# Optimization experiments

Hardware: AMD Instinct MI355X
Metric: run time of the kernel (lower is better)

## Reference

```python
import jax, jax.numpy as jnp
import numpy as np

IMAGE_C = 1
IMAGE_W = 28
PIXELS_PER_ROW = IMAGE_W * IMAGE_C  # 28

B, T, E = 16, IMAGE_W * IMAGE_W * IMAGE_C, 512  # T = 784
H = 8
D = E // H  # head_dim = 64


def get_2d_causal_bias(T):
    idx = jnp.arange(T)
    i = idx // PIXELS_PER_ROW          # row index
    j = (idx % PIXELS_PER_ROW) // IMAGE_C  # col index
    c = idx % IMAGE_C                  # channel index
    q_i, k_i = i[:, None], i[None, :]
    q_j, k_j = j[:, None], j[None, :]
    q_c, k_c = c[:, None], c[None, :]
    allowed = (k_i < q_i) | ((k_i == q_i) & (k_j < q_j)) | (
        (k_i == q_i) & (k_j == q_j) & (k_c <= q_c))
    bias = jnp.where(allowed, 0.0, -jnp.inf).astype(jnp.float32)
    return bias[None, None]  # [1, 1, T, T]


def setup_inputs() -> dict:
    key = jax.random.key(0)
    ks = jax.random.split(key, 5)
    s = 1.0 / np.sqrt(E)
    return {
        "x": jax.random.normal(ks[0], (B, T, E), dtype=jnp.float32),
        "Wq": jax.random.normal(ks[1], (E, E), dtype=jnp.float32) * s,
        "bq": jnp.zeros((E,), dtype=jnp.float32),
        "Wk": jax.random.normal(ks[2], (E, E), dtype=jnp.float32) * s,
        "bk": jnp.zeros((E,), dtype=jnp.float32),
        "Wv": jax.random.normal(ks[3], (E, E), dtype=jnp.float32) * s,
        "bv": jnp.zeros((E,), dtype=jnp.float32),
        "Wo": jax.random.normal(ks[4], (E, E), dtype=jnp.float32) * s,
        "bo": jnp.zeros((E,), dtype=jnp.float32),
    }


def reference(x, Wq, bq, Wk, bk, Wv, bv, Wo, bo):
    Bx, Tx, Ex = x.shape
    # projections (torch Linear: y = x @ W.T + b; here W stored as [E, E] used directly)
    Q = (x @ Wq + bq).reshape(Bx, Tx, H, D).transpose(0, 2, 1, 3)  # [B,H,T,D]
    K = (x @ Wk + bk).reshape(Bx, Tx, H, D).transpose(0, 2, 1, 3)
    V = (x @ Wv + bv).reshape(Bx, Tx, H, D).transpose(0, 2, 1, 3)
    scores = jnp.einsum("bhqd,bhkd->bhqk", Q, K) / jnp.sqrt(jnp.float32(D))
    scores = scores + get_2d_causal_bias(Tx)
    attn = jax.nn.softmax(scores, axis=-1)
    ctx = jnp.einsum("bhqk,bhkd->bhqd", attn, V)
    ctx = ctx.transpose(0, 2, 1, 3).reshape(Bx, Tx, Ex)
    return ctx @ Wo + bo
```

## Files before the change

kernel.cpp:

```cpp
#include <hip/hip_runtime.h>
#include <hip/hip_bf16.h>

#define BB    16
#define TT    784
#define TPK   832
#define TPQ   896
#define EE    512
#define HH    8
#define DD    64
#define BT    (BB*TT)

typedef short short8 __attribute__((ext_vector_type(8)));
typedef short short4v __attribute__((ext_vector_type(4)));
typedef float floatx4 __attribute__((ext_vector_type(4)));
typedef float floatx16 __attribute__((ext_vector_type(16)));
typedef unsigned uint4v __attribute__((ext_vector_type(4)));

__device__ __forceinline__ short f2bf(float f) {
    unsigned u = __builtin_bit_cast(unsigned, f);
    u += 0x7FFFu + ((u >> 16) & 1u);
    return (short)(u >> 16);
}

__device__ __forceinline__ unsigned cvtpk_bf16(float lo, float hi) {
    unsigned r;
    asm("v_cvt_pk_bf16_f32 %0, %1, %2" : "=v"(r) : "v"(lo), "v"(hi));
    return r;
}

__device__ __forceinline__ void gload_lds16(const short* g, short* l) {
    __builtin_amdgcn_global_load_lds(
        (const __attribute__((address_space(1))) void*)g,
        (__attribute__((address_space(3))) void*)l, 16, 0, 0);
}

__global__ void prep_kernel(const float* __restrict__ x, short* __restrict__ xb,
                            const float* __restrict__ Wq, const float* __restrict__ Wk,
                            const float* __restrict__ Wv, short* __restrict__ wqkvt,
                            const float* __restrict__ Wo, short* __restrict__ wot,
                            short* __restrict__ Qb, short* __restrict__ Kb, short* __restrict__ Vt)
{
    __shared__ short t[64][65];
    int b = blockIdx.x;
    if (b < 3136) {
        int i = (b * 256 + threadIdx.x) * 8;
        float4 a = *(const float4*)(x + i);
        float4 c = *(const float4*)(x + i + 4);
        short8 o;
        o[0] = f2bf(a.x); o[1] = f2bf(a.y); o[2] = f2bf(a.z); o[3] = f2bf(a.w);
        o[4] = f2bf(c.x); o[5] = f2bf(c.y); o[6] = f2bf(c.z); o[7] = f2bf(c.w);
        *(short8*)(xb + i) = o;
    } else if (b < 3392) {
        const float* W; short* out; int n0, k0;
        if (b < 3328) {
            int tt = b - 3136;
            n0 = (tt % 24) * 64; k0 = (tt / 24) * 64;
            W = (n0 < 512) ? Wq : (n0 < 1024 ? Wk : Wv);
            out = wqkvt;
        } else {
            int tt = b - 3328;
            n0 = (tt % 8) * 64; k0 = (tt / 8) * 64;
            W = Wo; out = wot;
        }
        int nn0 = n0 & 511;
        for (int i = threadIdx.x; i < 4096; i += 256) {
            int r = i >> 6, c = i & 63;
            t[r][c] = f2bf(W[(k0 + r) * 512 + nn0 + c]);
        }
        __syncthreads();
        for (int i = threadIdx.x; i < 4096; i += 256) {
            int nr = i >> 6, kc = i & 63;
            out[(n0 + nr) * 512 + k0 + kc] = t[kc][nr];
        }
    } else {
        int c = (b - 3392) * 256 + threadIdx.x;
        short8 z = (short8){0,0,0,0,0,0,0,0};
        if (c < 114688) {
            int bh = c / 896, j = c - bh * 896;
            *(short8*)&Qb[(bh * TPQ + TT) * 64 + j * 8] = z;
        } else if (c < 163840) {
            int c2 = c - 114688;
            int bh = c2 / 384, j = c2 - bh * 384;
            *(short8*)&Kb[(bh * TPK + TT) * 64 + j * 8] = z;
        } else {
            int c3 = c - 163840;
            int bh = c3 / 384, j = c3 - bh * 384;
            int d = j / 6, m = j - d * 6;
            *(short8*)&Vt[(bh * 64 + d) * TPK + TT + m * 8] = z;
        }
    }
}

__global__ __launch_bounds__(256, 4) void gemm_qkv_kernel(
    const short* __restrict__ A, const short* __restrict__ Bt,
    const float* __restrict__ bq, const float* __restrict__ bk, const float* __restrict__ bv,
    short* __restrict__ Qb, short* __restrict__ Kb, short* __restrict__ Vt)
{
    __shared__ __align__(16) short smem[16640];
    short* As0 = smem;
    short* Bs0 = smem + 8192;

    const int orig = blockIdx.x;
    const int tile = (orig & 7) * 147 + (orig >> 3);
    const int m0 = (tile / 12) * 128, n0 = (tile % 12) * 128;
    const int tid = threadIdx.x;
    const int lane = tid & 63, w = tid >> 6;
    const int wr = w >> 1, wc = w & 1;
    const int l16 = lane & 15, quad = lane >> 4;

    const int srow = w * 32 + (lane >> 2);
    const int scol = (lane & 3) * 8;
    const short* Ag = A  + (size_t)(m0 + srow) * 512 + scol;
    const short* Bg = Bt + (size_t)(n0 + srow) * 512 + scol;
    short* Abase = As0 + w * 1024;
    short* Bbase = Bs0 + w * 1024;

    auto stage = [&](int it) {
        int b = it & 1;
        int ko = it * 32;
        gload_lds16(Ag + ko,            Abase + b * 4096);
        gload_lds16(Ag + ko + 16 * 512, Abase + b * 4096 + 512);
        gload_lds16(Bg + ko,            Bbase + b * 4096);
        gload_lds16(Bg + ko + 16 * 512, Bbase + b * 4096 + 512);
    };

    floatx4 acc[4][4];
    #pragma unroll
    for (int i = 0; i < 4; i++)
        #pragma unroll
        for (int j = 0; j < 4; j++)
            acc[i][j] = (floatx4){0.f, 0.f, 0.f, 0.f};

    stage(0);
    __syncthreads();

    for (int it = 0; it < 16; it++) {
        if (it < 15) stage(it + 1);
        const short* as = As0 + (it & 1) * 4096;
        const short* bs = Bs0 + (it & 1) * 4096;
        short8 af[4], bf[4];
        #pragma unroll
        for (int i = 0; i < 4; i++) {
            af[i] = *(const short8*)&as[(wr * 64 + i * 16 + l16) * 32 + quad * 8];
            bf[i] = *(const short8*)&bs[(wc * 64 + i * 16 + l16) * 32 + quad * 8];
        }
        #pragma unroll
        for (int mi = 0; mi < 4; mi++)
            #pragma unroll
            for (int ni = 0; ni < 4; ni++)
                acc[mi][ni] = __builtin_amdgcn_mfma_f32_16x16x32_bf16(af[mi], bf[ni], acc[mi][ni], 0, 0, 0);
        __syncthreads();
    }

    const int sel = n0 >> 9;
    if (sel == 2) {
        #pragma unroll
        for (int mi = 0; mi < 4; mi++) {
            int m = m0 + wr * 64 + mi * 16 + quad * 4;
            int bb = m / TT, t = m - bb * TT;
            #pragma unroll
            for (int ni = 0; ni < 4; ni++) {
                int nn = (n0 + wc * 64 + ni * 16 + l16) & 511;
                int hh = nn >> 6, dd = nn & 63;
                float b = bv[nn];
                short4v pv;
                #pragma unroll
                for (int r = 0; r < 4; r++) pv[r] = f2bf(acc[mi][ni][r] + b);
                *(short4v*)&Vt[((size_t)(bb * HH + hh) * 64 + dd) * TPK + t] = pv;
            }
        }
    } else {
        short* Ct = smem;
        const float* bias = (sel == 0) ? bq : bk;
        #pragma unroll
        for (int mi = 0; mi < 4; mi++) {
            #pragma unroll
            for (int ni = 0; ni < 4; ni++) {
                int nl = wc * 64 + ni * 16 + l16;
                int nn = (n0 + nl) & 511;
                float b = bias[nn];
                #pragma unroll
                for (int r = 0; r < 4; r++) {
                    float v = acc[mi][ni][r] + b;
                    if (sel == 0) v *= 0.125f;
                    Ct[(wr * 64 + mi * 16 + quad * 4 + r) * 130 + nl] = f2bf(v);
                }
            }
        }
        __syncthreads();
        short* dst = (sel == 0) ? Qb : Kb;
        const int tp = (sel == 0) ? TPQ : TPK;
        int nl = lane * 2;
        int nn = (n0 + nl) & 511;
        int hh = nn >> 6, dd = nn & 63;
        #pragma unroll 4
        for (int rr = 0; rr < 32; rr++) {
            int ml = w * 32 + rr;
            int m = m0 + ml;
            int bb = m / TT, t = m - bb * TT;
            unsigned pv = *(const unsigned*)&Ct[ml * 130 + nl];
            *(unsigned*)&dst[((bb * HH + hh) * tp + t) * 64 + dd] = pv;
        }
    }
}

__global__ __launch_bounds__(256, 3) void attn_kernel(
    const short* __restrict__ Qb, const short* __restrict__ Kb, const short* __restrict__ Vt,
    short* __restrict__ ctx)
{
    const int g = blockIdx.x;
    const int low = g & 7, rest = g >> 3;
    const int qt = 12 - (rest >> 4);
    const int bh = ((rest & 15) << 3) | low;
    const int bb = bh >> 3, hh = bh & 7;
    const int tid = threadIdx.x;
    const int lane = tid & 63, w = tid >> 6;
    const int wq = w >> 1, wk = w & 1;
    const int l32 = lane & 31, hi = lane >> 5;
    const int r7 = l32 & 7;

    __shared__ __align__(16) short Ks[2][4096];
    __shared__ __align__(16) short Vs[2][4096];

    const short* Kbase = Kb + (size_t)(bh * TPK) * 64;
    const short* Vbase = Vt + (size_t)(bh * 64) * TPK;

    const int srow = tid >> 3;
    const int sc8  = tid & 7;
    const int scol = sc8 * 8;
    const int ksw  = (sc8 ^ (srow & 7)) * 8;
    const int vg0  = (sc8 >> 1) * 2;
    const int vsw0 = ((vg0       ^ (srow & 7)) * 8) + (sc8 & 1) * 4;
    const int vsw1 = (((vg0 + 1) ^ (srow & 7)) * 8) + (sc8 & 1) * 4;

    short8 kreg[2], vreg[2];
    auto load_tile = [&](int kt) {
        #pragma unroll
        for (int p = 0; p < 2; p++) {
            int row = srow + p * 32;
            kreg[p] = *(const short8*)(Kbase + (kt * 64 + row) * 64 + scol);
            vreg[p] = *(const short8*)(Vbase + row * TPK + kt * 64 + scol);
        }
    };
    auto store_tile = [&](int b) {
        #pragma unroll
        for (int p = 0; p < 2; p++) {
            int ro = (srow + p * 32) * 64;
            *(short8*)&Ks[b][ro + ksw] = kreg[p];
            short4v v0, v1;
            #pragma unroll
            for (int i = 0; i < 4; i++) { v0[i] = vreg[p][i]; v1[i] = vreg[p][i + 4]; }
            *(short4v*)&Vs[b][ro + vsw0] = v0;
            *(short4v*)&Vs[b][ro + vsw1] = v1;
        }
    };

    const int q_lo = qt * 64 + wq * 32;
    const int qg = q_lo + l32;
    const bool wreal = (q_lo < TT);
    const short* Qrow = Qb + (size_t)(bh * TPQ + qg) * 64;
    short8 qf[4];
    #pragma unroll
    for (int d = 0; d < 4; d++) qf[d] = *(const short8*)(Qrow + d * 16 + hi * 8);

    floatx16 accO[2];
    #pragma unroll
    for (int dt = 0; dt < 2; dt++)
        #pragma unroll
        for (int i = 0; i < 16; i++) accO[dt][i] = 0.f;
    float accL = 0.f;

    load_tile(0);
    store_tile(0);

    for (int kt = 0; kt <= qt; kt++) {
        const int cb = kt & 1;
        if (kt < qt) load_tile(kt + 1);
        __syncthreads();
        const int kbase = kt * 64 + wk * 32;
        if (wreal && kbase <= q_lo + 31) {
            floatx16 z;
            #pragma unroll
            for (int i = 0; i < 16; i++) z[i] = 0.f;
            #pragma unroll
            for (int d = 0; d < 4; d++) {
                short8 kf = *(const short8*)&Ks[cb][(wk * 32 + l32) * 64 + (((d * 2 + hi) ^ r7) * 8)];
                z = __builtin_amdgcn_mfma_f32_32x32x16_bf16(kf, qf[d], z, 0, 0, 0);
            }
            float p[16];
            #pragma unroll
            for (int r = 0; r < 16; r++) p[r] = __expf(z[r]);
            if (kbase + 31 > q_lo) {
                #pragma unroll
                for (int r = 0; r < 16; r++) {
                    int keyg = kbase + (r & 3) + 8 * (r >> 2) + 4 * hi;
                    if (keyg > qg) p[r] = 0.f;
                }
            }
            #pragma unroll
            for (int r = 0; r < 16; r++) accL += p[r];
            #pragma unroll
            for (int s = 0; s < 2; s++) {
                uint4v pw;
                #pragma unroll
                for (int jj = 0; jj < 4; jj++)
                    pw[jj] = cvtpk_bf16(p[8 * s + 2 * jj], p[8 * s + 2 * jj + 1]);
                short8 pb = __builtin_bit_cast(short8, pw);
                #pragma unroll
                for (int dt = 0; dt < 2; dt++) {
                    short8 vf = *(const short8*)&Vs[cb][(dt * 32 + l32) * 64 + (((wk * 4 + s * 2 + hi) ^ r7) * 8)];
                    accO[dt] = __builtin_amdgcn_mfma_f32_32x32x16_bf16(vf, pb, accO[dt], 0, 0, 0);
                }
            }
        }
        if (kt < qt) store_tile((kt + 1) & 1);
    }

    __syncthreads();
    float* rbuf  = (float*)&Ks[0][0];
    float* rbufL = (float*)&Vs[0][0];
    if (wk == 1) {
        #pragma unroll
        for (int dt = 0; dt < 2; dt++)
            #pragma unroll
            for (int r = 0; r < 16; r++)
                rbuf[((wq * 2 + dt) * 16 + r) * 64 + lane] = accO[dt][r];
        rbufL[wq * 64 + lane] = accL;
    }
    __syncthreads();
    if (wk == 0) {
        #pragma unroll
        for (int dt = 0; dt < 2; dt++)
            #pragma unroll
            for (int r = 0; r < 16; r++)
                accO[dt][r] += rbuf[((wq * 2 + dt) * 16 + r) * 64 + lane];
        accL += rbufL[wq * 64 + lane];
        float Lt = accL + __shfl_xor(accL, 32, 64);
        if (wreal && qg < TT) {
            float inv = 1.f / Lt;
            short* crow = ctx + (size_t)(bb * TT + qg) * 512 + hh * 64;
            #pragma unroll
            for (int dt = 0; dt < 2; dt++)
                #pragma unroll
                for (int g4 = 0; g4 < 4; g4++) {
                    short4v pv;
                    #pragma unroll
                    for (int r4 = 0; r4 < 4; r4++) pv[r4] = f2bf(accO[dt][g4 * 4 + r4] * inv);
                    *(short4v*)&crow[dt * 32 + g4 * 8 + 4 * hi] = pv;
                }
        }
    }
}

__global__ __launch_bounds__(256, 4) void gemm_out_kernel(
    const short* __restrict__ A, const short* __restrict__ Bt,
    const float* __restrict__ bo, float* __restrict__ out)
{
    __shared__ __align__(16) short smem[16384];
    short* As0 = smem;
    short* Bs0 = smem + 8192;

    const int orig = blockIdx.x;
    const int tile = (orig & 7) * 49 + (orig >> 3);
    const int m0 = (tile >> 2) * 128, n0 = (tile & 3) * 128;
    const int tid = threadIdx.x;
    const int lane = tid & 63, w = tid >> 6;
    const int wr = w >> 1, wc = w & 1;
    const int l16 = lane & 15, quad = lane >> 4;

    const int srow = w * 32 + (lane >> 2);
    const int scol = (lane & 3) * 8;
    const short* Ag = A  + (size_t)(m0 + srow) * 512 + scol;
    const short* Bg = Bt + (size_t)(n0 + srow) * 512 + scol;
    short* Abase = As0 + w * 1024;
    short* Bbase = Bs0 + w * 1024;

    auto stage = [&](int it) {
        int b = it & 1;
        int ko = it * 32;
        gload_lds16(Ag + ko,            Abase + b * 4096);
        gload_lds16(Ag + ko + 16 * 512, Abase + b * 4096 + 512);
        gload_lds16(Bg + ko,            Bbase + b * 4096);
        gload_lds16(Bg + ko + 16 * 512, Bbase + b * 4096 + 512);
    };

    floatx4 acc[4][4];
    #pragma unroll
    for (int i = 0; i < 4; i++)
        #pragma unroll
        for (int j = 0; j < 4; j++)
            acc[i][j] = (floatx4){0.f, 0.f, 0.f, 0.f};

    stage(0);
    __syncthreads();

    for (int it = 0; it < 16; it++) {
        if (it < 15) stage(it + 1);
        const short* as = As0 + (it & 1) * 4096;
        const short* bs = Bs0 + (it & 1) * 4096;
        short8 af[4], bf[4];
        #pragma unroll
        for (int i = 0; i < 4; i++) {
            af[i] = *(const short8*)&as[(wr * 64 + i * 16 + l16) * 32 + quad * 8];
            bf[i] = *(const short8*)&bs[(wc * 64 + i * 16 + l16) * 32 + quad * 8];
        }
        #pragma unroll
        for (int mi = 0; mi < 4; mi++)
            #pragma unroll
            for (int ni = 0; ni < 4; ni++)
                acc[mi][ni] = __builtin_amdgcn_mfma_f32_16x16x32_bf16(af[mi], bf[ni], acc[mi][ni], 0, 0, 0);
        __syncthreads();
    }

    #pragma unroll
    for (int mi = 0; mi < 4; mi++) {
        #pragma unroll
        for (int ni = 0; ni < 4; ni++) {
            int n = n0 + wc * 64 + ni * 16 + l16;
            float bias = bo[n];
            #pragma unroll
            for (int r = 0; r < 4; r++) {
                int m = m0 + wr * 64 + mi * 16 + quad * 4 + r;
                out[(size_t)m * 512 + n] = acc[mi][ni][r] + bias;
            }
        }
    }
}

extern "C" void kernel_launch(void* const* d_in, const int* in_sizes, int n_in,
                              void* d_out, int out_size, void* d_ws, size_t ws_size,
                              hipStream_t stream) {
    const float* x  = (const float*)d_in[0];
    const float* Wq = (const float*)d_in[1];
    const float* bq = (const float*)d_in[2];
    const float* Wk = (const float*)d_in[3];
    const float* bk = (const float*)d_in[4];
    const float* Wv = (const float*)d_in[5];
    const float* bv = (const float*)d_in[6];
    const float* Wo = (const float*)d_in[7];
    const float* bo = (const float*)d_in[8];
    float* out = (float*)d_out;

    char* ws = (char*)d_ws;
    size_t off = 0;
    auto alloc = [&](size_t bytes) -> void* {
        void* p = ws + off;
        off += (bytes + 255) & ~(size_t)255;
        return p;
    };
    short* xb    = (short*)alloc((size_t)BT * EE * 2);
    short* wqkvt = (short*)alloc((size_t)1536 * 512 * 2);
    short* wot   = (short*)alloc((size_t)512 * 512 * 2);
    short* Qb    = (short*)alloc((size_t)BB * HH * TPQ * DD * 2);
    short* Kb    = (short*)alloc((size_t)BB * HH * TPK * DD * 2);
    short* Vtb   = (short*)alloc((size_t)BB * HH * DD * TPK * 2);
    short* ctxb  = (short*)alloc((size_t)BT * EE * 2);

    prep_kernel<<<4224, 256, 0, stream>>>(x, xb, Wq, Wk, Wv, wqkvt, Wo, wot, Qb, Kb, Vtb);
    gemm_qkv_kernel<<<1176, 256, 0, stream>>>(xb, wqkvt, bq, bk, bv, Qb, Kb, Vtb);
    attn_kernel<<<1664, 256, 0, stream>>>(Qb, Kb, Vtb, ctxb);
    gemm_out_kernel<<<392, 256, 0, stream>>>(ctxb, wot, bo, out);
}
```

Baseline: 160.4 us.

## Triple-buffer QKV GEMM loads with vmcnt waits and k-major LDS layout

Moves the QKV projection GEMM from double to triple buffering in LDS. Loads are prefetched two stages ahead, and completion is tracked with explicit s_waitcnt vmcnt plus one barrier per iteration instead of two __syncthreads. The LDS tile layout changes to k-chunk-major, which alters how threads map to global loads and likely reduces LDS bank conflicts on the fragment reads. In exchange, LDS use grows and launch bounds drop to 3 blocks per CU, which reduces occupancy.

```diff
diff --git a/kernel.cpp b/kernel.cpp
--- a/kernel.cpp
+++ b/kernel.cpp
@@ -91,14 +91,14 @@
     }
 }
 
-__global__ __launch_bounds__(256, 4) void gemm_qkv_kernel(
+__global__ __launch_bounds__(256, 3) void gemm_qkv_kernel(
     const short* __restrict__ A, const short* __restrict__ Bt,
     const float* __restrict__ bq, const float* __restrict__ bk, const float* __restrict__ bv,
     short* __restrict__ Qb, short* __restrict__ Kb, short* __restrict__ Vt)
 {
-    __shared__ __align__(16) short smem[16640];
+    __shared__ __align__(16) short smem[24576];
     short* As0 = smem;
-    short* Bs0 = smem + 8192;
+    short* Bs0 = smem + 12288;
 
     const int orig = blockIdx.x;
     const int tile = (orig & 7) * 147 + (orig >> 3);
@@ -108,20 +108,18 @@
     const int wr = w >> 1, wc = w & 1;
     const int l16 = lane & 15, quad = lane >> 4;
 
-    const int srow = w * 32 + (lane >> 2);
-    const int scol = (lane & 3) * 8;
-    const short* Ag = A  + (size_t)(m0 + srow) * 512 + scol;
-    const short* Bg = Bt + (size_t)(n0 + srow) * 512 + scol;
-    short* Abase = As0 + w * 1024;
-    short* Bbase = Bs0 + w * 1024;
+    const int sr = tid & 127;
+    const int sc = tid >> 7;
+    const short* Ag = A  + (size_t)(m0 + sr) * 512 + sc * 8;
+    const short* Bg = Bt + (size_t)(n0 + sr) * 512 + sc * 8;
 
     auto stage = [&](int it) {
-        int b = it & 1;
+        int b = it % 3;
         int ko = it * 32;
-        gload_lds16(Ag + ko,            Abase + b * 4096);
-        gload_lds16(Ag + ko + 16 * 512, Abase + b * 4096 + 512);
-        gload_lds16(Bg + ko,            Bbase + b * 4096);
-        gload_lds16(Bg + ko + 16 * 512, Bbase + b * 4096 + 512);
+        gload_lds16(Ag + ko,      As0 + b * 4096 + tid * 8);
+        gload_lds16(Ag + ko + 16, As0 + b * 4096 + 2048 + tid * 8);
+        gload_lds16(Bg + ko,      Bs0 + b * 4096 + tid * 8);
+        gload_lds16(Bg + ko + 16, Bs0 + b * 4096 + 2048 + tid * 8);
     };
 
     floatx4 acc[4][4];
@@ -132,25 +130,30 @@
             acc[i][j] = (floatx4){0.f, 0.f, 0.f, 0.f};
 
     stage(0);
-    __syncthreads();
-
+    stage(1);
+
+    #pragma unroll
     for (int it = 0; it < 16; it++) {
-        if (it < 15) stage(it + 1);
-        const short* as = As0 + (it & 1) * 4096;
-        const short* bs = Bs0 + (it & 1) * 4096;
+        if (it < 15) asm volatile("s_waitcnt vmcnt(4)" ::: "memory");
+        else         asm volatile("s_waitcnt vmcnt(0)" ::: "memory");
+        __builtin_amdgcn_s_barrier();
+        __builtin_amdgcn_sched_barrier(0);
+        if (it < 14) stage(it + 2);
+        const short* as = As0 + (it % 3) * 4096;
+        const short* bs = Bs0 + (it % 3) * 4096;
         short8 af[4], bf[4];
         #pragma unroll
         for (int i = 0; i < 4; i++) {
-            af[i] = *(const short8*)&as[(wr * 64 + i * 16 + l16) * 32 + quad * 8];
-            bf[i] = *(const short8*)&bs[(wc * 64 + i * 16 + l16) * 32 + quad * 8];
+            af[i] = *(const short8*)&as[quad * 1024 + (wr * 64 + i * 16 + l16) * 8];
+            bf[i] = *(const short8*)&bs[quad * 1024 + (wc * 64 + i * 16 + l16) * 8];
         }
         #pragma unroll
         for (int mi = 0; mi < 4; mi++)
             #pragma unroll
             for (int ni = 0; ni < 4; ni++)
                 acc[mi][ni] = __builtin_amdgcn_mfma_f32_16x16x32_bf16(af[mi], bf[ni], acc[mi][ni], 0, 0, 0);
-        __syncthreads();
-    }
+    }
+    __syncthreads();
 
     const int sel = n0 >> 9;
     if (sel == 2) {
```

Result: slower. 174.4 us (+8.8%).

## Give each attention wave its own query rows over a 128-row block

Applied to the files above, without the earlier changes.

The attention kernel now processes 128 query rows per block, with each of the four waves owning 32 query rows and looping over both 32-key halves of every K/V tile. Before, pairs of waves split the keys and combined results through shared memory. The change removes that cross-wave reduction and its two barriers, and roughly halves how often K/V tiles are loaded per query. In exchange the grid shrinks from 1664 to 896 blocks, so there is less parallelism and coarser causal load balance. Each wave also does more serial work per tile.

```diff
diff --git a/kernel.cpp b/kernel.cpp
--- a/kernel.cpp
+++ b/kernel.cpp
@@ -210,12 +210,11 @@
 {
     const int g = blockIdx.x;
     const int low = g & 7, rest = g >> 3;
-    const int qt = 12 - (rest >> 4);
+    const int qb = 6 - (rest >> 4);
     const int bh = ((rest & 15) << 3) | low;
     const int bb = bh >> 3, hh = bh & 7;
     const int tid = threadIdx.x;
     const int lane = tid & 63, w = tid >> 6;
-    const int wq = w >> 1, wk = w & 1;
     const int l32 = lane & 31, hi = lane >> 5;
     const int r7 = l32 & 7;
 
@@ -255,9 +254,13 @@
         }
     };
 
-    const int q_lo = qt * 64 + wq * 32;
-    const int qg = q_lo + l32;
+    const int q0   = qb * 128;
+    const int q_lo = q0 + w * 32;
+    const int qg   = q_lo + l32;
     const bool wreal = (q_lo < TT);
+    const int q_top = (q0 + 127 < TT - 1) ? (q0 + 127) : (TT - 1);
+    const int KT = (q_top >> 6) + 1;
+
     const short* Qrow = Qb + (size_t)(bh * TPQ + qg) * 64;
     short8 qf[4];
     #pragma unroll
@@ -273,82 +276,66 @@
     load_tile(0);
     store_tile(0);
 
-    for (int kt = 0; kt <= qt; kt++) {
+    for (int kt = 0; kt < KT; kt++) {
         const int cb = kt & 1;
-        if (kt < qt) load_tile(kt + 1);
+        if (kt < KT - 1) load_tile(kt + 1);
         __syncthreads();
-        const int kbase = kt * 64 + wk * 32;
-        if (wreal && kbase <= q_lo + 31) {
-            floatx16 z;
-            #pragma unroll
-            for (int i = 0; i < 16; i++) z[i] = 0.f;
-            #pragma unroll
-            for (int d = 0; d < 4; d++) {
-                short8 kf = *(const short8*)&Ks[cb][(wk * 32 + l32) * 64 + (((d * 2 + hi) ^ r7) * 8)];
-                z = __builtin_amdgcn_mfma_f32_32x32x16_bf16(kf, qf[d], z, 0, 0, 0);
-            }
-            float p[16];
-            #pragma unroll
-            for (int r = 0; r < 16; r++) p[r] = __expf(z[r]);
-            if (kbase + 31 > q_lo) {
-                #pragma unroll
-                for (int r = 0; r < 16; r++) {
-                    int keyg = kbase + (r & 3) + 8 * (r >> 2) + 4 * hi;
-                    if (keyg > qg) p[r] = 0.f;
+        if (wreal) {
+            #pragma unroll
+            for (int kh = 0; kh < 2; kh++) {
+                const int kbase = kt * 64 + kh * 32;
+                if (kbase > q_lo + 31) continue;
+                floatx16 z;
+                #pragma unroll
+                for (int i = 0; i < 16; i++) z[i] = 0.f;
+                #pragma unroll
+                for (int d = 0; d < 4; d++) {
+                    short8 kf = *(const short8*)&Ks[cb][(kh * 32 + l32) * 64 + (((d * 2 + hi) ^ r7) * 8)];
+                    z = __builtin_amdgcn_mfma_f32_32x32x16_bf16(kf, qf[d], z, 0, 0, 0);
+                }
+                float p[16];
+                #pragma unroll
+                for (int r = 0; r < 16; r++) p[r] = __expf(z[r]);
+                if (kbase + 31 > q_lo) {
+                    #pragma unroll
+                    for (int r = 0; r < 16; r++) {
+                        int keyg = kbase + (r & 3) + 8 * (r >> 2) + 4 * hi;
+                        if (keyg > qg) p[r] = 0.f;
+                    }
+                }
+                #pragma unroll
+                for (int r = 0; r < 16; r++) accL += p[r];
+                #pragma unroll
+                for (int s = 0; s < 2; s++) {
+                    uint4v pw;
+                    #pragma unroll
+                    for (int jj = 0; jj < 4; jj++)
+                        pw[jj] = cvtpk_bf16(p[8 * s + 2 * jj], p[8 * s + 2 * jj + 1]);
+                    short8 pb = __builtin_bit_cast(short8, pw);
+                    #pragma unroll
+                    for (int dt = 0; dt < 2; dt++) {
+                        short8 vf = *(const short8*)&Vs[cb][(dt * 32 + l32) * 64 + (((kh * 4 + s * 2 + hi) ^ r7) * 8)];
+                        accO[dt] = __builtin_amdgcn_mfma_f32_32x32x16_bf16(vf, pb, accO[dt], 0, 0, 0);
+                    }
                 }
             }
-            #pragma unroll
-            for (int r = 0; r < 16; r++) accL += p[r];
-            #pragma unroll
-            for (int s = 0; s < 2; s++) {
-                uint4v pw;
-                #pragma unroll
-                for (int jj = 0; jj < 4; jj++)
-                    pw[jj] = cvtpk_bf16(p[8 * s + 2 * jj], p[8 * s + 2 * jj + 1]);
-                short8 pb = __builtin_bit_cast(short8, pw);
-                #pragma unroll
-                for (int dt = 0; dt < 2; dt++) {
-                    short8 vf = *(const short8*)&Vs[cb][(dt * 32 + l32) * 64 + (((wk * 4 + s * 2 + hi) ^ r7) * 8)];
-                    accO[dt] = __builtin_amdgcn_mfma_f32_32x32x16_bf16(vf, pb, accO[dt], 0, 0, 0);
-                }
+        }
+        if (kt < KT - 1) store_tile((kt + 1) & 1);
+    }
+
+    float Lt = accL + __shfl_xor(accL, 32, 64);
+    if (wreal && qg < TT) {
+        float inv = 1.f / Lt;
+        short* crow = ctx + (size_t)(bb * TT + qg) * 512 + hh * 64;
+        #pragma unroll
+        for (int dt = 0; dt < 2; dt++)
+            #pragma unroll
+            for (int g4 = 0; g4 < 4; g4++) {
+                short4v pv;
+                #pragma unroll
+                for (int r4 = 0; r4 < 4; r4++) pv[r4] = f2bf(accO[dt][g4 * 4 + r4] * inv);
+                *(short4v*)&crow[dt * 32 + g4 * 8 + 4 * hi] = pv;
             }
-        }
-        if (kt < qt) store_tile((kt + 1) & 1);
-    }
-
-    __syncthreads();
-    float* rbuf  = (float*)&Ks[0][0];
-    float* rbufL = (float*)&Vs[0][0];
-    if (wk == 1) {
-        #pragma unroll
-        for (int dt = 0; dt < 2; dt++)
-            #pragma unroll
-            for (int r = 0; r < 16; r++)
-                rbuf[((wq * 2 + dt) * 16 + r) * 64 + lane] = accO[dt][r];
-        rbufL[wq * 64 + lane] = accL;
-    }
-    __syncthreads();
-    if (wk == 0) {
-        #pragma unroll
-        for (int dt = 0; dt < 2; dt++)
-            #pragma unroll
-            for (int r = 0; r < 16; r++)
-                accO[dt][r] += rbuf[((wq * 2 + dt) * 16 + r) * 64 + lane];
-        accL += rbufL[wq * 64 + lane];
-        float Lt = accL + __shfl_xor(accL, 32, 64);
-        if (wreal && qg < TT) {
-            float inv = 1.f / Lt;
-            short* crow = ctx + (size_t)(bb * TT + qg) * 512 + hh * 64;
-            #pragma unroll
-            for (int dt = 0; dt < 2; dt++)
-                #pragma unroll
-                for (int g4 = 0; g4 < 4; g4++) {
-                    short4v pv;
-                    #pragma unroll
-                    for (int r4 = 0; r4 < 4; r4++) pv[r4] = f2bf(accO[dt][g4 * 4 + r4] * inv);
-                    *(short4v*)&crow[dt * 32 + g4 * 8 + 4 * hi] = pv;
-                }
-        }
     }
 }
 
@@ -458,6 +445,6 @@
 
     prep_kernel<<<4224, 256, 0, stream>>>(x, xb, Wq, Wk, Wv, wqkvt, Wo, wot, Qb, Kb, Vtb);
     gemm_qkv_kernel<<<1176, 256, 0, stream>>>(xb, wqkvt, bq, bk, bv, Qb, Kb, Vtb);
-    attn_kernel<<<1664, 256, 0, stream>>>(Qb, Kb, Vtb, ctxb);
+    attn_kernel<<<896, 256, 0, stream>>>(Qb, Kb, Vtb, ctxb);
     gemm_out_kernel<<<392, 256, 0, stream>>>(ctxb, wot, bo, out);
 }
```

Measured after the change: 158.1 us. About the same (-1.4%).
